# Kernel tuning notes

Measured on AMD Instinct MI355X. Metric: run time of the kernel, lower is better.

Reference implementation:

```python
import jax, jax.numpy as jnp
import numpy as np

RNN_DIMS = 1024
FC_DIMS = 1024
N_CLASSES = 256
BATCH = 128


def setup_inputs() -> dict:
    key = jax.random.key(0)
    ks = jax.random.split(key, 10)
    s = 1.0 / np.sqrt(RNN_DIMS)
    inp = {
        "x": jax.random.normal(ks[0], (BATCH, RNN_DIMS), dtype=jnp.float32),
        "h1": jax.random.normal(ks[1], (BATCH, RNN_DIMS), dtype=jnp.float32),
        # GRUCell params (PyTorch layout: [3*H, H] stacked as r,z,n)
        "w_ih": jax.random.uniform(ks[2], (3 * RNN_DIMS, RNN_DIMS), jnp.float32, -s, s),
        "w_hh": jax.random.uniform(ks[3], (3 * RNN_DIMS, RNN_DIMS), jnp.float32, -s, s),
        "b_ih": jax.random.uniform(ks[4], (3 * RNN_DIMS,), jnp.float32, -s, s),
        "b_hh": jax.random.uniform(ks[5], (3 * RNN_DIMS,), jnp.float32, -s, s),
        "w_fc1": jax.random.uniform(ks[6], (FC_DIMS, RNN_DIMS), jnp.float32, -s, s),
        "b_fc1": jax.random.uniform(ks[7], (FC_DIMS,), jnp.float32, -s, s),
        "w_fc3": jax.random.uniform(ks[8], (N_CLASSES, FC_DIMS), jnp.float32, -1.0 / np.sqrt(FC_DIMS), 1.0 / np.sqrt(FC_DIMS)),
        "b_fc3": jax.random.uniform(ks[9], (N_CLASSES,), jnp.float32, -1.0 / np.sqrt(FC_DIMS), 1.0 / np.sqrt(FC_DIMS)),
    }
    return inp


def reference(x, h1, w_ih, w_hh, b_ih, b_hh, w_fc1, b_fc1, w_fc3, b_fc3):
    # --- GRUCell (PyTorch semantics) ---
    gi = x @ w_ih.T + b_ih          # [B, 3H]
    gh = h1 @ w_hh.T + b_hh         # [B, 3H]
    i_r, i_z, i_n = jnp.split(gi, 3, axis=-1)
    h_r, h_z, h_n = jnp.split(gh, 3, axis=-1)
    r = jax.nn.sigmoid(i_r + h_r)
    z = jax.nn.sigmoid(i_z + h_z)
    n = jnp.tanh(i_n + r * h_n)
    h1_prime = (1.0 - z) * n + z * h1   # [B, H]
    # --- residual + MLP head ---
    res = h1_prime + x
    relu1 = jax.nn.relu(res @ w_fc1.T + b_fc1)   # [B, FC]
    out = relu1 @ w_fc3.T + b_fc3                # [B, N_CLASSES]
    return (out, h1_prime)
```

## Files before the change

### kernel.cpp

```cpp
#include <hip/hip_runtime.h>
#include <math.h>

typedef short bf16x8 __attribute__((ext_vector_type(8)));
typedef float f32x4 __attribute__((ext_vector_type(4)));

__device__ __forceinline__ int cvt2(float lo, float hi) {
    int r;
    asm("v_cvt_pk_bf16_f32 %0, %1, %2" : "=v"(r) : "v"(lo), "v"(hi));
    return r;
}

#define BAR() do {                                                        \
        asm volatile("s_waitcnt lgkmcnt(0)" ::: "memory");                \
        __builtin_amdgcn_s_barrier();                                     \
        __builtin_amdgcn_sched_barrier(0);                                \
    } while (0)

__global__ __launch_bounds__(256, 2) void gates_k(
    const float* __restrict__ x, const float* __restrict__ h1,
    const float* __restrict__ w_ih, const float* __restrict__ w_hh,
    const float* __restrict__ b_ih, const float* __restrict__ b_hh,
    float* __restrict__ h1p, float* __restrict__ res,
    float* __restrict__ zf1p, float* __restrict__ zout)
{
    __shared__ short As[2][64 * 64];
    __shared__ short Ws[2][96 * 64];
    const int tid  = threadIdx.x;
    const int lane = tid & 63;
    const int wv   = tid >> 6;
    const int b    = blockIdx.x;

    if (tid < 128) { f32x4 z = {}; *(f32x4*)(zf1p + b * 512 + tid * 4) = z; }
    if (tid < 32)  { f32x4 z = {}; *(f32x4*)(zout + b * 128 + tid * 4) = z; }

    const int tile = b & 63;
    const int rgq  = b >> 6;
    const int c0   = tile * 16;
    const int row0 = rgq * 32;
    const int r0 = tid >> 3, kc = tid & 7;

    const float* aP[2] = { x  + (row0 + r0) * 1024 + kc * 8,
                           h1 + (row0 + r0) * 1024 + kc * 8 };
    const int saI[2] = { (r0 * 64 + kc * 8) ^ ((r0 & 7) << 3),
                         ((r0 + 32) * 64 + kc * 8) ^ ((r0 & 7) << 3) };
    const float* wP[3];
    int swI[3];
    #pragma unroll
    for (int i = 0; i < 3; ++i) {
        int mw = r0 + 32 * i;
        int g = mw >> 4;
        const float* src = (g < 3) ? w_ih : w_hh;
        wP[i] = src + ((g % 3) * 1024 + c0 + (mw & 15)) * 1024 + kc * 8;
        swI[i] = (mw * 64 + kc * 8) ^ ((mw & 7) << 3);
    }

    f32x4 A[2][2][2], W[2][3][2];
    f32x4 acc[3] = {};

    const int rowg = wv & 1;
    const int hsel = wv >> 1;
    const int gbase = hsel * 3;

#define G_ISSUE(kt, s) do {                                               \
        _Pragma("unroll")                                                 \
        for (int i = 0; i < 2; ++i) {                                     \
            A[s][i][0] = *(const f32x4*)(aP[i] + (kt) * 64);              \
            A[s][i][1] = *(const f32x4*)(aP[i] + (kt) * 64 + 4);          \
        }                                                                 \
        _Pragma("unroll")                                                 \
        for (int i = 0; i < 3; ++i) {                                     \
            W[s][i][0] = *(const f32x4*)(wP[i] + (kt) * 64);              \
            W[s][i][1] = *(const f32x4*)(wP[i] + (kt) * 64 + 4);          \
        }                                                                 \
    } while (0)

#define G_STAGE(s, bb) do {                                               \
        _Pragma("unroll")                                                 \
        for (int i = 0; i < 2; ++i) {                                     \
            int4 p;                                                       \
            p.x = cvt2(A[s][i][0][0], A[s][i][0][1]);                     \
            p.y = cvt2(A[s][i][0][2], A[s][i][0][3]);                     \
            p.z = cvt2(A[s][i][1][0], A[s][i][1][1]);                     \
            p.w = cvt2(A[s][i][1][2], A[s][i][1][3]);                     \
            *(int4*)&As[bb][saI[i]] = p;                                  \
        }                                                                 \
        _Pragma("unroll")                                                 \
        for (int i = 0; i < 3; ++i) {                                     \
            int4 q;                                                       \
            q.x = cvt2(W[s][i][0][0], W[s][i][0][1]);                     \
            q.y = cvt2(W[s][i][0][2], W[s][i][0][3]);                     \
            q.z = cvt2(W[s][i][1][0], W[s][i][1][1]);                     \
            q.w = cvt2(W[s][i][1][2], W[s][i][1][3]);                     \
            *(int4*)&Ws[bb][swI[i]] = q;                                  \
        }                                                                 \
    } while (0)

#define G_COMPUTE(bb) do {                                                \
        _Pragma("unroll")                                                 \
        for (int kk = 0; kk < 64; kk += 32) {                             \
            const int kw = kk + 8 * (lane >> 4);                          \
            const int ma = hsel * 32 + rowg * 16 + (lane & 15);           \
            bf16x8 af = *(const bf16x8*)&As[bb][(ma * 64 + kw) ^ ((ma & 7) << 3)]; \
            _Pragma("unroll")                                             \
            for (int gg = 0; gg < 3; ++gg) {                              \
                int br = (gbase + gg) * 16 + (lane & 15);                 \
                bf16x8 bw = *(const bf16x8*)&Ws[bb][(br * 64 + kw) ^ ((br & 7) << 3)]; \
                acc[gg] = __builtin_amdgcn_mfma_f32_16x16x32_bf16(        \
                    af, bw, acc[gg], 0, 0, 0);                            \
            }                                                             \
        }                                                                 \
    } while (0)

    G_ISSUE(0, 0); G_ISSUE(1, 1);
    #pragma unroll 1
    for (int kt2 = 0; kt2 < 8; ++kt2) {
        const int kt = 2 * kt2;
        G_STAGE(0, 0); if (kt + 2 < 16) G_ISSUE(kt + 2, 0); BAR(); G_COMPUTE(0);
        G_STAGE(1, 1); if (kt + 3 < 16) G_ISSUE(kt + 3, 1); BAR(); G_COMPUTE(1);
    }
#undef G_ISSUE
#undef G_STAGE
#undef G_COMPUTE

    float* xch = (float*)&As[0][0];
    if (hsel) {
        #pragma unroll
        for (int gg = 0; gg < 3; ++gg)
            #pragma unroll
            for (int r = 0; r < 4; ++r)
                xch[(rowg * 3 + gg) * 256 + ((lane >> 4) * 4 + r) * 16 + (lane & 15)]
                    = acc[gg][r];
    }
    BAR();
    if (!hsel) {
        const int j = c0 + (lane & 15);
        const float bir = b_ih[j], biz = b_ih[1024 + j], bin = b_ih[2048 + j];
        const float bhr = b_hh[j], bhz = b_hh[1024 + j], bhn = b_hh[2048 + j];
        const int rbase = row0 + rowg * 16 + (lane >> 4) * 4;
        #pragma unroll
        for (int r = 0; r < 4; ++r) {
            const int row = rbase + r;
            const int xb  = rowg * 3 * 256 + ((lane >> 4) * 4 + r) * 16 + (lane & 15);
            float ir  = acc[0][r] + bir, iz = acc[1][r] + biz, inn = acc[2][r] + bin;
            float hr  = xch[xb] + bhr, hz = xch[xb + 256] + bhz, hn = xch[xb + 512] + bhn;
            float rr = 1.0f / (1.0f + __expf(-(ir + hr)));
            float zz = 1.0f / (1.0f + __expf(-(iz + hz)));
            float nn = tanhf(inn + rr * hn);
            float h1v = h1[row * 1024 + j];
            float hp  = (1.0f - zz) * nn + zz * h1v;
            h1p[row * 1024 + j] = hp;
            res[row * 1024 + j] = hp + x[row * 1024 + j];
        }
    }
}

template<int NT, bool ATOMIC, bool RELUA>
__global__ __launch_bounds__(256, 2) void gemm_k(
    const float* __restrict__ act, const float* __restrict__ wgt,
    const float* __restrict__ bias,
    float* __restrict__ out, int ldo, int nkt, int ksbits)
{
    constexpr int CT = NT / 16;
    __shared__ short As[2][64 * 64];
    __shared__ short Ws[2][NT * 64];

    const int tid  = threadIdx.x;
    const int lane = tid & 63;
    const int wv   = tid >> 6;

    const int ks   = blockIdx.x & ((1 << ksbits) - 1);
    const int rest = blockIdx.x >> ksbits;
    const int rg   = rest & 1;
    const int tile = rest >> 1;
    const int c0   = tile * NT;
    const int row0 = rg * 64;
    const int kt0  = ks * nkt;

    const int r0 = tid >> 3, kc = tid & 7;
    const float* aP = act + (row0 + r0) * 1024 + kt0 * 64 + kc * 8;
    const float* wP = wgt + (c0 + r0) * 1024 + kt0 * 64 + kc * 8;
    const bool wAct = (tid < NT * 8);

    const int saI0 = (r0 * 64 + kc * 8) ^ ((r0 & 7) << 3);
    const int saI1 = ((r0 + 32) * 64 + kc * 8) ^ ((r0 & 7) << 3);

    f32x4 A[4][4], W[4][2];
    f32x4 acc[CT] = {};

#define ISSUE(kt, s) do {                                                 \
        A[s][0] = *(const f32x4*)(aP + (kt) * 64);                        \
        A[s][1] = *(const f32x4*)(aP + (kt) * 64 + 4);                    \
        A[s][2] = *(const f32x4*)(aP + (kt) * 64 + 32768);                \
        A[s][3] = *(const f32x4*)(aP + (kt) * 64 + 32772);                \
        if (wAct) {                                                       \
            W[s][0] = *(const f32x4*)(wP + (kt) * 64);                    \
            W[s][1] = *(const f32x4*)(wP + (kt) * 64 + 4);                \
        }                                                                 \
    } while (0)

#define RL(v) (RELUA ? fmaxf((v), 0.0f) : (v))

#define STAGE(s, b) do {                                                  \
        int4 p0, p1;                                                      \
        p0.x = cvt2(RL(A[s][0][0]), RL(A[s][0][1]));                      \
        p0.y = cvt2(RL(A[s][0][2]), RL(A[s][0][3]));                      \
        p0.z = cvt2(RL(A[s][1][0]), RL(A[s][1][1]));                      \
        p0.w = cvt2(RL(A[s][1][2]), RL(A[s][1][3]));                      \
        p1.x = cvt2(RL(A[s][2][0]), RL(A[s][2][1]));                      \
        p1.y = cvt2(RL(A[s][2][2]), RL(A[s][2][3]));                      \
        p1.z = cvt2(RL(A[s][3][0]), RL(A[s][3][1]));                      \
        p1.w = cvt2(RL(A[s][3][2]), RL(A[s][3][3]));                      \
        *(int4*)&As[b][saI0] = p0;                                        \
        *(int4*)&As[b][saI1] = p1;                                        \
        if (wAct) {                                                       \
            int4 q;                                                       \
            q.x = cvt2(W[s][0][0], W[s][0][1]);                           \
            q.y = cvt2(W[s][0][2], W[s][0][3]);                           \
            q.z = cvt2(W[s][1][0], W[s][1][1]);                           \
            q.w = cvt2(W[s][1][2], W[s][1][3]);                           \
            *(int4*)&Ws[b][saI0] = q;                                     \
        }                                                                 \
    } while (0)

#define COMPUTE(b) do {                                                   \
        _Pragma("unroll")                                                 \
        for (int kk = 0; kk < 64; kk += 32) {                             \
            const int kw = kk + 8 * (lane >> 4);                          \
            const int ar = wv * 16 + (lane & 15);                         \
            bf16x8 af = *(const bf16x8*)&As[b][(ar * 64 + kw) ^ ((ar & 7) << 3)]; \
            bf16x8 bw[CT];                                                \
            _Pragma("unroll")                                             \
            for (int ct = 0; ct < CT; ++ct) {                             \
                int br = ct * 16 + (lane & 15);                           \
                bw[ct] = *(const bf16x8*)&Ws[b][(br * 64 + kw) ^ ((br & 7) << 3)]; \
            }                                                             \
            _Pragma("unroll")                                             \
            for (int ct = 0; ct < CT; ++ct)                               \
                acc[ct] = __builtin_amdgcn_mfma_f32_16x16x32_bf16(        \
                    af, bw[ct], acc[ct], 0, 0, 0);                        \
        }                                                                 \
    } while (0)

    ISSUE(0, 0); ISSUE(1, 1); ISSUE(2, 2); ISSUE(3, 3);

    #pragma unroll 1
    for (int g = 0; g < nkt / 4; ++g) {
        const int kt = 4 * g;
        STAGE(0, 0); if (kt + 4 < nkt) ISSUE(kt + 4, 0); BAR(); COMPUTE(0);
        STAGE(1, 1); if (kt + 5 < nkt) ISSUE(kt + 5, 1); BAR(); COMPUTE(1);
        STAGE(2, 0); if (kt + 6 < nkt) ISSUE(kt + 6, 2); BAR(); COMPUTE(0);
        STAGE(3, 1); if (kt + 7 < nkt) ISSUE(kt + 7, 3); BAR(); COMPUTE(1);
    }

#undef ISSUE
#undef RL
#undef STAGE
#undef COMPUTE

    #pragma unroll
    for (int ct = 0; ct < CT; ++ct) {
        int col = c0 + ct * 16 + (lane & 15);
        float bv = (bias && ks == 0) ? bias[col] : 0.0f;
        #pragma unroll
        for (int r = 0; r < 4; ++r) {
            int row = row0 + wv * 16 + (lane >> 4) * 4 + r;
            float v = acc[ct][r] + bv;
            if (ATOMIC) unsafeAtomicAdd(&out[row * ldo + col], v);
            else        out[row * ldo + col] = v;
        }
    }
}

extern "C" void kernel_launch(void* const* d_in, const int* in_sizes, int n_in,
                              void* d_out, int out_size, void* d_ws, size_t ws_size,
                              hipStream_t stream)
{
    const float* x     = (const float*)d_in[0];
    const float* h1    = (const float*)d_in[1];
    const float* w_ih  = (const float*)d_in[2];
    const float* w_hh  = (const float*)d_in[3];
    const float* b_ih  = (const float*)d_in[4];
    const float* b_hh  = (const float*)d_in[5];
    const float* w_fc1 = (const float*)d_in[6];
    const float* b_fc1 = (const float*)d_in[7];
    const float* w_fc3 = (const float*)d_in[8];
    const float* b_fc3 = (const float*)d_in[9];

    float* out = (float*)d_out;
    float* h1p = out + 128 * 256;

    float* ws  = (float*)d_ws;
    float* res = ws;
    float* f1p = ws + 128 * 1024;

    gates_k<<<256, 256, 0, stream>>>(x, h1, w_ih, w_hh, b_ih, b_hh,
                                     h1p, res, f1p, out);
    gemm_k<16, true, false><<<512, 256, 0, stream>>>(
        res, w_fc1, b_fc1, f1p, 1024, 4, 2);
    gemm_k<16, true, true><<<128, 256, 0, stream>>>(
        f1p, w_fc3, b_fc3, out, 256, 4, 2);
}
```

Before: 25.45 us.

## Load GRU activation fragments directly into registers, bypassing shared-memory staging

```diff
diff --git a/kernel.cpp b/kernel.cpp
--- a/kernel.cpp
+++ b/kernel.cpp
@@ -23,7 +23,6 @@
     float* __restrict__ h1p, float* __restrict__ res,
     float* __restrict__ zf1p, float* __restrict__ zout)
 {
-    __shared__ short As[2][64 * 64];
     __shared__ short Ws[2][96 * 64];
     const int tid  = threadIdx.x;
     const int lane = tid & 63;
@@ -39,10 +38,14 @@
     const int row0 = rgq * 32;
     const int r0 = tid >> 3, kc = tid & 7;
 
-    const float* aP[2] = { x  + (row0 + r0) * 1024 + kc * 8,
-                           h1 + (row0 + r0) * 1024 + kc * 8 };
-    const int saI[2] = { (r0 * 64 + kc * 8) ^ ((r0 & 7) << 3),
-                         ((r0 + 32) * 64 + kc * 8) ^ ((r0 & 7) << 3) };
+    const int rowg = wv & 1;
+    const int hsel = wv >> 1;
+    const int gbase = hsel * 3;
+
+    const float* aF = (hsel ? h1 : x)
+                      + (row0 + rowg * 16 + (lane & 15)) * 1024
+                      + 8 * (lane >> 4);
+
     const float* wP[3];
     int swI[3];
     #pragma unroll
@@ -54,19 +57,18 @@
         swI[i] = (mw * 64 + kc * 8) ^ ((mw & 7) << 3);
     }
 
-    f32x4 A[2][2][2], W[2][3][2];
+    f32x4 Ar[2][2][2];
+    f32x4 W[2][3][2];
     f32x4 acc[3] = {};
 
-    const int rowg = wv & 1;
-    const int hsel = wv >> 1;
-    const int gbase = hsel * 3;
-
-#define G_ISSUE(kt, s) do {                                               \
-        _Pragma("unroll")                                                 \
-        for (int i = 0; i < 2; ++i) {                                     \
-            A[s][i][0] = *(const f32x4*)(aP[i] + (kt) * 64);              \
-            A[s][i][1] = *(const f32x4*)(aP[i] + (kt) * 64 + 4);          \
-        }                                                                 \
+#define G_ISSUE_A(kt, s) do {                                             \
+        Ar[s][0][0] = *(const f32x4*)(aF + (kt) * 64);                    \
+        Ar[s][0][1] = *(const f32x4*)(aF + (kt) * 64 + 4);                \
+        Ar[s][1][0] = *(const f32x4*)(aF + (kt) * 64 + 32);               \
+        Ar[s][1][1] = *(const f32x4*)(aF + (kt) * 64 + 36);               \
+    } while (0)
+
+#define G_ISSUE_W(kt, s) do {                                             \
         _Pragma("unroll")                                                 \
         for (int i = 0; i < 3; ++i) {                                     \
             W[s][i][0] = *(const f32x4*)(wP[i] + (kt) * 64);              \
@@ -74,16 +76,7 @@
         }                                                                 \
     } while (0)
 
-#define G_STAGE(s, bb) do {                                               \
-        _Pragma("unroll")                                                 \
-        for (int i = 0; i < 2; ++i) {                                     \
-            int4 p;                                                       \
-            p.x = cvt2(A[s][i][0][0], A[s][i][0][1]);                     \
-            p.y = cvt2(A[s][i][0][2], A[s][i][0][3]);                     \
-            p.z = cvt2(A[s][i][1][0], A[s][i][1][1]);                     \
-            p.w = cvt2(A[s][i][1][2], A[s][i][1][3]);                     \
-            *(int4*)&As[bb][saI[i]] = p;                                  \
-        }                                                                 \
+#define G_STAGE_W(s, bb) do {                                             \
         _Pragma("unroll")                                                 \
         for (int i = 0; i < 3; ++i) {                                     \
             int4 q;                                                       \
@@ -95,12 +88,16 @@
         }                                                                 \
     } while (0)
 
-#define G_COMPUTE(bb) do {                                                \
+#define G_COMPUTE(s, bb) do {                                             \
         _Pragma("unroll")                                                 \
-        for (int kk = 0; kk < 64; kk += 32) {                             \
-            const int kw = kk + 8 * (lane >> 4);                          \
-            const int ma = hsel * 32 + rowg * 16 + (lane & 15);           \
-            bf16x8 af = *(const bf16x8*)&As[bb][(ma * 64 + kw) ^ ((ma & 7) << 3)]; \
+        for (int kk2 = 0; kk2 < 2; ++kk2) {                               \
+            const int kw = kk2 * 32 + 8 * (lane >> 4);                    \
+            int4 pa;                                                      \
+            pa.x = cvt2(Ar[s][kk2][0][0], Ar[s][kk2][0][1]);              \
+            pa.y = cvt2(Ar[s][kk2][0][2], Ar[s][kk2][0][3]);              \
+            pa.z = cvt2(Ar[s][kk2][1][0], Ar[s][kk2][1][1]);              \
+            pa.w = cvt2(Ar[s][kk2][1][2], Ar[s][kk2][1][3]);              \
+            bf16x8 af = *(bf16x8*)&pa;                                    \
             _Pragma("unroll")                                             \
             for (int gg = 0; gg < 3; ++gg) {                              \
                 int br = (gbase + gg) * 16 + (lane & 15);                 \
@@ -111,18 +108,25 @@
         }                                                                 \
     } while (0)
 
-    G_ISSUE(0, 0); G_ISSUE(1, 1);
+    G_ISSUE_A(0, 0); G_ISSUE_A(1, 1);
+    G_ISSUE_W(0, 0); G_ISSUE_W(1, 1);
+
     #pragma unroll 1
     for (int kt2 = 0; kt2 < 8; ++kt2) {
         const int kt = 2 * kt2;
-        G_STAGE(0, 0); if (kt + 2 < 16) G_ISSUE(kt + 2, 0); BAR(); G_COMPUTE(0);
-        G_STAGE(1, 1); if (kt + 3 < 16) G_ISSUE(kt + 3, 1); BAR(); G_COMPUTE(1);
-    }
-#undef G_ISSUE
-#undef G_STAGE
+        G_STAGE_W(0, 0); if (kt + 2 < 16) G_ISSUE_W(kt + 2, 0);
+        BAR();
+        G_COMPUTE(0, 0); if (kt + 2 < 16) G_ISSUE_A(kt + 2, 0);
+        G_STAGE_W(1, 1); if (kt + 3 < 16) G_ISSUE_W(kt + 3, 1);
+        BAR();
+        G_COMPUTE(1, 1); if (kt + 3 < 16) G_ISSUE_A(kt + 3, 1);
+    }
+#undef G_ISSUE_A
+#undef G_ISSUE_W
+#undef G_STAGE_W
 #undef G_COMPUTE
 
-    float* xch = (float*)&As[0][0];
+    float* xch = (float*)&Ws[0][0];
     if (hsel) {
         #pragma unroll
         for (int gg = 0; gg < 3; ++gg)
```

Result: slower. 27.65 us (+8.6%).

## Split gates GEMM along K into two halves and add separate GRU epilogue kernel

Applied to the files above, without the earlier changes.

```diff
diff --git a/kernel.cpp b/kernel.cpp
--- a/kernel.cpp
+++ b/kernel.cpp
@@ -19,8 +19,7 @@
 __global__ __launch_bounds__(256, 2) void gates_k(
     const float* __restrict__ x, const float* __restrict__ h1,
     const float* __restrict__ w_ih, const float* __restrict__ w_hh,
-    const float* __restrict__ b_ih, const float* __restrict__ b_hh,
-    float* __restrict__ h1p, float* __restrict__ res,
+    float* __restrict__ gbuf,
     float* __restrict__ zf1p, float* __restrict__ zout)
 {
     __shared__ short As[2][64 * 64];
@@ -30,13 +29,17 @@
     const int wv   = tid >> 6;
     const int b    = blockIdx.x;
 
-    if (tid < 128) { f32x4 z = {}; *(f32x4*)(zf1p + b * 512 + tid * 4) = z; }
-    if (tid < 32)  { f32x4 z = {}; *(f32x4*)(zout + b * 128 + tid * 4) = z; }
+    if (b < 256) {
+        if (tid < 128) { f32x4 z = {}; *(f32x4*)(zf1p + b * 512 + tid * 4) = z; }
+        if (tid < 32)  { f32x4 z = {}; *(f32x4*)(zout + b * 128 + tid * 4) = z; }
+    }
 
     const int tile = b & 63;
-    const int rgq  = b >> 6;
+    const int rgq  = (b >> 6) & 3;
+    const int ks   = b >> 8;
     const int c0   = tile * 16;
     const int row0 = rgq * 32;
+    const int kt0  = ks * 8;
     const int r0 = tid >> 3, kc = tid & 7;
 
     const float* aP[2] = { x  + (row0 + r0) * 1024 + kc * 8,
@@ -111,47 +114,54 @@
         }                                                                 \
     } while (0)
 
-    G_ISSUE(0, 0); G_ISSUE(1, 1);
+    G_ISSUE(kt0 + 0, 0); G_ISSUE(kt0 + 1, 1);
     #pragma unroll 1
-    for (int kt2 = 0; kt2 < 8; ++kt2) {
-        const int kt = 2 * kt2;
-        G_STAGE(0, 0); if (kt + 2 < 16) G_ISSUE(kt + 2, 0); BAR(); G_COMPUTE(0);
-        G_STAGE(1, 1); if (kt + 3 < 16) G_ISSUE(kt + 3, 1); BAR(); G_COMPUTE(1);
+    for (int kt2 = 0; kt2 < 4; ++kt2) {
+        const int kt = kt0 + 2 * kt2;
+        G_STAGE(0, 0); if (kt + 2 < kt0 + 8) G_ISSUE(kt + 2, 0); BAR(); G_COMPUTE(0);
+        G_STAGE(1, 1); if (kt + 3 < kt0 + 8) G_ISSUE(kt + 3, 1); BAR(); G_COMPUTE(1);
     }
 #undef G_ISSUE
 #undef G_STAGE
 #undef G_COMPUTE
 
-    float* xch = (float*)&As[0][0];
-    if (hsel) {
+    const int j = c0 + (lane & 15);
+    const int rbase = row0 + rowg * 16 + (lane >> 4) * 4;
+    float* gb = gbuf + ks * 6 * 131072;
+    #pragma unroll
+    for (int gg = 0; gg < 3; ++gg) {
+        float* gp = gb + (gbase + gg) * 131072;
         #pragma unroll
-        for (int gg = 0; gg < 3; ++gg)
-            #pragma unroll
-            for (int r = 0; r < 4; ++r)
-                xch[(rowg * 3 + gg) * 256 + ((lane >> 4) * 4 + r) * 16 + (lane & 15)]
-                    = acc[gg][r];
-    }
-    BAR();
-    if (!hsel) {
-        const int j = c0 + (lane & 15);
-        const float bir = b_ih[j], biz = b_ih[1024 + j], bin = b_ih[2048 + j];
-        const float bhr = b_hh[j], bhz = b_hh[1024 + j], bhn = b_hh[2048 + j];
-        const int rbase = row0 + rowg * 16 + (lane >> 4) * 4;
-        #pragma unroll
-        for (int r = 0; r < 4; ++r) {
-            const int row = rbase + r;
-            const int xb  = rowg * 3 * 256 + ((lane >> 4) * 4 + r) * 16 + (lane & 15);
-            float ir  = acc[0][r] + bir, iz = acc[1][r] + biz, inn = acc[2][r] + bin;
-            float hr  = xch[xb] + bhr, hz = xch[xb + 256] + bhz, hn = xch[xb + 512] + bhn;
-            float rr = 1.0f / (1.0f + __expf(-(ir + hr)));
-            float zz = 1.0f / (1.0f + __expf(-(iz + hz)));
-            float nn = tanhf(inn + rr * hn);
-            float h1v = h1[row * 1024 + j];
-            float hp  = (1.0f - zz) * nn + zz * h1v;
-            h1p[row * 1024 + j] = hp;
-            res[row * 1024 + j] = hp + x[row * 1024 + j];
-        }
-    }
+        for (int r = 0; r < 4; ++r)
+            gp[(rbase + r) * 1024 + j] = acc[gg][r];
+    }
+}
+
+__global__ __launch_bounds__(256) void gru_k(
+    const float* __restrict__ gbuf, const float* __restrict__ x,
+    const float* __restrict__ h1,
+    const float* __restrict__ b_ih, const float* __restrict__ b_hh,
+    float* __restrict__ h1p, float* __restrict__ res)
+{
+    int id = blockIdx.x * 256 + threadIdx.x;
+    int j = id & 1023;
+    float g_[6];
+    #pragma unroll
+    for (int gi = 0; gi < 6; ++gi)
+        g_[gi] = gbuf[gi * 131072 + id] + gbuf[(6 + gi) * 131072 + id];
+    float ir  = g_[0] + b_ih[j];
+    float iz  = g_[1] + b_ih[1024 + j];
+    float inn = g_[2] + b_ih[2048 + j];
+    float hr  = g_[3] + b_hh[j];
+    float hz  = g_[4] + b_hh[1024 + j];
+    float hn  = g_[5] + b_hh[2048 + j];
+    float rr = 1.0f / (1.0f + __expf(-(ir + hr)));
+    float zz = 1.0f / (1.0f + __expf(-(iz + hz)));
+    float nn = tanhf(inn + rr * hn);
+    float h1v = h1[id];
+    float hp  = (1.0f - zz) * nn + zz * h1v;
+    h1p[id] = hp;
+    res[id] = hp + x[id];
 }
 
 template<int NT, bool ATOMIC, bool RELUA>
@@ -289,12 +299,13 @@
     float* out = (float*)d_out;
     float* h1p = out + 128 * 256;
 
-    float* ws  = (float*)d_ws;
-    float* res = ws;
-    float* f1p = ws + 128 * 1024;
-
-    gates_k<<<256, 256, 0, stream>>>(x, h1, w_ih, w_hh, b_ih, b_hh,
-                                     h1p, res, f1p, out);
+    float* ws   = (float*)d_ws;
+    float* res  = ws;
+    float* f1p  = ws + 128 * 1024;
+    float* gbuf = ws + 256 * 1024;
+
+    gates_k<<<512, 256, 0, stream>>>(x, h1, w_ih, w_hh, gbuf, f1p, out);
+    gru_k<<<512, 256, 0, stream>>>(gbuf, x, h1, b_ih, b_hh, h1p, res);
     gemm_k<16, true, false><<<512, 256, 0, stream>>>(
         res, w_fc1, b_fc1, f1p, 1024, 4, 2);
     gemm_k<16, true, true><<<128, 256, 0, stream>>>(
```

New measurement: 26.68 us. 1.05x slower.
